# Kernel optimization log

Hardware: AMD Instinct MI355X
Metric: run time of the kernel (lower is better)

The kernel has to match this reference:

```python
import jax, jax.numpy as jnp
import numpy as np

V, D, MAXLEN, B, C = 32000, 1024, 2048, 4, 2048


def setup_inputs() -> dict:
    key = jax.random.key(0)
    ks = jax.random.split(key, 8)
    x = jax.random.randint(ks[0], (B, C), 0, V, dtype=jnp.int64)
    s = 0.02
    embed = jax.random.normal(ks[1], (V, D), dtype=jnp.float32) * s
    pe = jax.random.normal(ks[2], (MAXLEN, D), dtype=jnp.float32) * s
    Wq = jax.random.normal(ks[3], (D, D), dtype=jnp.float32) * s
    Wk = jax.random.normal(ks[4], (D, D), dtype=jnp.float32) * s
    Wv = jax.random.normal(ks[5], (D, D), dtype=jnp.float32) * s
    Wo = jax.random.normal(ks[6], (V, D), dtype=jnp.float32) * s
    bo = jnp.zeros((V,), dtype=jnp.float32)
    return {"x": x, "embed": embed, "pe": pe, "Wq": Wq, "Wk": Wk, "Wv": Wv, "Wo": Wo, "bo": bo}


def reference(x, embed, pe, Wq, Wk, Wv, Wo, bo):
    Bc, Cc = x.shape
    Dd = embed.shape[1]
    # token embedding + learned absolute PE (pos_offset = 0)
    h = embed[x] + pe[:Cc]                      # (B, C, D)
    # single-head Q/K/V projections (torch Linear: y = x @ W.T)
    Q = jnp.einsum('bcd,ed->bce', h, Wq)
    K = jnp.einsum('bcd,ed->bce', h, Wk)
    Vv = jnp.einsum('bcd,ed->bce', h, Wv)
    scores = jnp.einsum('bqd,bkd->bqk', Q, K) / jnp.sqrt(jnp.float32(Dd))
    # additive causal mask: 0 on lower triangle, -inf above
    mask = jnp.where(jnp.tril(jnp.ones((Cc, Cc), dtype=bool)), 0.0, -jnp.inf).astype(scores.dtype)
    weights = jax.nn.softmax(scores + mask, axis=-1)  # (B, C, C)
    attn_out = jnp.einsum('bqk,bkd->bqd', weights, Vv)
    hidden = h + attn_out
    logits = jnp.einsum('bcd,vd->bcv', hidden, Wo) + bo
    return logits
```

## Files before the change

### kernel.cpp

```cpp
#include <hip/hip_runtime.h>

#define DEV __device__ __forceinline__

typedef __attribute__((ext_vector_type(8))) __bf16 bf16x8;
typedef __attribute__((ext_vector_type(4))) float f32x4;

DEV unsigned short f2bf(float f) {
    unsigned u = __builtin_bit_cast(unsigned, f);
    u += 0x7fffu + ((u >> 16) & 1u);
    return (unsigned short)(u >> 16);
}
DEV float bf2f(unsigned short s) {
    unsigned u = ((unsigned)s) << 16;
    return __builtin_bit_cast(float, u);
}

DEV void gload_lds16(const unsigned short* g, unsigned short* l) {
    __builtin_amdgcn_global_load_lds(
        (const __attribute__((address_space(1))) unsigned int*)g,
        (__attribute__((address_space(3))) unsigned int*)l, 16, 0, 0);
}


__global__ __launch_bounds__(256) void k_cast_bf16(const float* __restrict__ src,
                                                   unsigned short* __restrict__ dst, int n4) {
    int i = blockIdx.x * 256 + threadIdx.x;
    if (i >= n4) return;
    float4 v = reinterpret_cast<const float4*>(src)[i];
    ushort4 o;
    o.x = f2bf(v.x); o.y = f2bf(v.y); o.z = f2bf(v.z); o.w = f2bf(v.w);
    reinterpret_cast<ushort4*>(dst)[i] = o;
}

__global__ __launch_bounds__(256) void k_cast3(const float* __restrict__ a,
                                               const float* __restrict__ b,
                                               const float* __restrict__ c,
                                               unsigned short* __restrict__ oa,
                                               unsigned short* __restrict__ ob,
                                               unsigned short* __restrict__ oc,
                                               int n4each) {
    int i = blockIdx.x * 256 + threadIdx.x;
    int w = i / n4each, j = i - w * n4each;
    const float* s = (w == 0) ? a : (w == 1) ? b : c;
    unsigned short* d = (w == 0) ? oa : (w == 1) ? ob : oc;
    float4 v = reinterpret_cast<const float4*>(s)[j];
    ushort4 o;
    o.x = f2bf(v.x); o.y = f2bf(v.y); o.z = f2bf(v.z); o.w = f2bf(v.w);
    reinterpret_cast<ushort4*>(d)[j] = o;
}

__global__ __launch_bounds__(256) void k_prep_h(const int* __restrict__ x,
                                                const float* __restrict__ embed,
                                                const float* __restrict__ pe,
                                                unsigned short* __restrict__ h) {
    const int r = blockIdx.x;
    const int pos = r & 2047;
    const int tok = x[r];
    const int t = threadIdx.x;
    float4 e = reinterpret_cast<const float4*>(embed + (size_t)tok * 1024)[t];
    float4 p = reinterpret_cast<const float4*>(pe + (size_t)pos * 1024)[t];
    ushort4 o;
    o.x = f2bf(e.x + p.x); o.y = f2bf(e.y + p.y);
    o.z = f2bf(e.z + p.z); o.w = f2bf(e.w + p.w);
    reinterpret_cast<ushort4*>(h + (size_t)r * 1024)[t] = o;
}

__global__ __launch_bounds__(256) void k_softmax_causal(const float* __restrict__ S,
                                                        unsigned short* __restrict__ W) {
    const int r = blockIdx.x;
    const int q = r & 2047;
    const float* row = S + (size_t)r * 2048;
    unsigned short* orow = W + (size_t)r * 2048;
    const int t = threadIdx.x;
    const float scale = 0.03125f;
    const int kceil4 = (((q >> 7) + 1) << 7) >> 2;
    float p[8];
    float mx = -1e30f;
    #pragma unroll
    for (int i = 0; i < 2; ++i) {
        int i4 = t + i * 256;
        int base = i4 * 4;
        float4 v = (float4){0.f, 0.f, 0.f, 0.f};
        if (base <= q) v = reinterpret_cast<const float4*>(row)[i4];
        p[i*4+0] = (base+0 <= q) ? v.x * scale : -1e30f;
        p[i*4+1] = (base+1 <= q) ? v.y * scale : -1e30f;
        p[i*4+2] = (base+2 <= q) ? v.z * scale : -1e30f;
        p[i*4+3] = (base+3 <= q) ? v.w * scale : -1e30f;
        #pragma unroll
        for (int j = 0; j < 4; ++j) mx = fmaxf(mx, p[i*4+j]);
    }
    #pragma unroll
    for (int o = 32; o > 0; o >>= 1) mx = fmaxf(mx, __shfl_xor(mx, o));
    __shared__ float redm[4];
    __shared__ float reds[4];
    const int w = t >> 6;
    if ((t & 63) == 0) redm[w] = mx;
    __syncthreads();
    mx = fmaxf(fmaxf(redm[0], redm[1]), fmaxf(redm[2], redm[3]));
    float e[8];
    float s = 0.f;
    #pragma unroll
    for (int i = 0; i < 8; ++i) { e[i] = __expf(p[i] - mx); s += e[i]; }
    #pragma unroll
    for (int o = 32; o > 0; o >>= 1) s += __shfl_xor(s, o);
    if ((t & 63) == 0) reds[w] = s;
    __syncthreads();
    s = (reds[0] + reds[1]) + (reds[2] + reds[3]);
    const float inv = 1.0f / s;
    #pragma unroll
    for (int i = 0; i < 2; ++i) {
        int i4 = t + i * 256;
        if (i4 < kceil4) {
            ushort4 o4;
            o4.x = f2bf(e[i*4+0] * inv);
            o4.y = f2bf(e[i*4+1] * inv);
            o4.z = f2bf(e[i*4+2] * inv);
            o4.w = f2bf(e[i*4+3] * inv);
            reinterpret_cast<ushort4*>(orow)[i4] = o4;
        }
    }
}

template<int OUT_BF16, int TRANS_OUT, int ADD_BIAS, int ADD_RES, int CAUSAL_SKIP, int TRI_K>
__global__ __launch_bounds__(256)
void k_gemm_bt(const unsigned short* __restrict__ A,
               const unsigned short* __restrict__ B,
               void* __restrict__ Out,
               const float* __restrict__ bias,
               const unsigned short* __restrict__ Res,
               int M, int N, int K, int ldo,
               long long sA, long long sB, long long sC, long long sRes) {
    const int bm = blockIdx.x, bn = blockIdx.y, bz = blockIdx.z;
    if (CAUSAL_SKIP && bn > bm) return;
    A += (long long)bz * sA;
    B += (long long)bz * sB;

    __shared__ __align__(16) unsigned short As[128 * 32];
    __shared__ __align__(16) unsigned short Bs[128 * 32];

    const int t = threadIdx.x;
    const int w = t >> 6;
    const int lane = t & 63;
    const int wm = w >> 1, wn = w & 1;
    const int fr = lane & 15, fq = lane >> 4;

    f32x4 acc[4][4];
    #pragma unroll
    for (int mi = 0; mi < 4; ++mi)
        #pragma unroll
        for (int ni = 0; ni < 4; ++ni)
            acc[mi][ni] = (f32x4){0.f, 0.f, 0.f, 0.f};

    const int kend = TRI_K ? ((K < (bm + 1) * 128) ? K : (bm + 1) * 128) : K;

    const int c0 = t, c1 = t + 256;
    const unsigned short* gA0 = A + (size_t)(bm * 128 + (c0 >> 2)) * K + (c0 & 3) * 8;
    const unsigned short* gA1 = A + (size_t)(bm * 128 + (c1 >> 2)) * K + (c1 & 3) * 8;
    const unsigned short* gB0 = B + (size_t)(bn * 128 + (c0 >> 2)) * K + (c0 & 3) * 8;
    const unsigned short* gB1 = B + (size_t)(bn * 128 + (c1 >> 2)) * K + (c1 & 3) * 8;
    unsigned short* lA0 = As + w * 512;
    unsigned short* lA1 = As + 2048 + w * 512;
    unsigned short* lB0 = Bs + w * 512;
    unsigned short* lB1 = Bs + 2048 + w * 512;

    for (int kt = 0; kt < kend; kt += 32) {
        gload_lds16(gA0 + kt, lA0);
        gload_lds16(gA1 + kt, lA1);
        gload_lds16(gB0 + kt, lB0);
        gload_lds16(gB1 + kt, lB1);
        __syncthreads();

        bf16x8 af[4], bfr[4];
        #pragma unroll
        for (int mi = 0; mi < 4; ++mi)
            af[mi] = *reinterpret_cast<const bf16x8*>(As + (wm * 64 + mi * 16 + fr) * 32 + fq * 8);
        #pragma unroll
        for (int ni = 0; ni < 4; ++ni)
            bfr[ni] = *reinterpret_cast<const bf16x8*>(Bs + (wn * 64 + ni * 16 + fr) * 32 + fq * 8);
        #pragma unroll
        for (int mi = 0; mi < 4; ++mi)
            #pragma unroll
            for (int ni = 0; ni < 4; ++ni)
                acc[mi][ni] = __builtin_amdgcn_mfma_f32_16x16x32_bf16(af[mi], bfr[ni], acc[mi][ni], 0, 0, 0);
        __syncthreads();
    }

    const int row0 = bm * 128 + wm * 64 + fq * 4;
    const int col0 = bn * 128 + wn * 64 + fr;
    if (OUT_BF16) {
        unsigned short* O = (unsigned short*)Out + (long long)bz * sC;
        #pragma unroll
        for (int mi = 0; mi < 4; ++mi) {
            #pragma unroll
            for (int j = 0; j < 4; ++j) {
                const int row = row0 + mi * 16 + j;
                unsigned short* orow = O + (size_t)row * ldo;
                const unsigned short* rrow =
                    ADD_RES ? (Res + (long long)bz * sRes + (size_t)row * ldo) : (const unsigned short*)nullptr;
                #pragma unroll
                for (int ni = 0; ni < 4; ++ni) {
                    const int col = col0 + ni * 16;
                    float v = acc[mi][ni][j];
                    if (ADD_RES) v += bf2f(rrow[col]);
                    orow[col] = f2bf(v);
                }
            }
        }
    } else {
        float* O = (float*)Out + (long long)bz * sC;
        #pragma unroll
        for (int mi = 0; mi < 4; ++mi) {
            #pragma unroll
            for (int j = 0; j < 4; ++j) {
                const int row = row0 + mi * 16 + j;
                float* orow = O + (size_t)row * ldo;
                #pragma unroll
                for (int ni = 0; ni < 4; ++ni) {
                    const int col = col0 + ni * 16;
                    float v = acc[mi][ni][j];
                    if (ADD_BIAS) v += bias[col];
                    orow[col] = v;
                }
            }
        }
    }
}


#define SA3(buf, kt) do { \
    unsigned short* d_ = Lds + (buf)*16384 + w*512; \
    gload_lds16(gA0 + (kt)*32, d_); \
    gload_lds16(gA1 + (kt)*32, d_ + 4096); } while(0)

#define SB3(buf, kt) do { \
    unsigned short* d_ = Lds + (buf)*16384 + 8192 + w*512; \
    gload_lds16(gB0 + (kt)*32, d_); \
    gload_lds16(gB1 + (kt)*32, d_ + 4096); } while(0)

#define LDA3(buf, mi) (*reinterpret_cast<const bf16x8*>(Lds + (buf)*16384 + aBase + (mi)*512))
#define LDB3(buf, ni) (*reinterpret_cast<const bf16x8*>(Lds + (buf)*16384 + 8192 + bBase + (ni)*512))

#define MF16(arow, af) do { \
    __builtin_amdgcn_s_setprio(1); \
    _Pragma("unroll") \
    for (int j_ = 0; j_ < 4; ++j_) \
        _Pragma("unroll") \
        for (int n_ = 0; n_ < 4; ++n_) \
            acc[(arow)+j_][n_] = __builtin_amdgcn_mfma_f32_16x16x32_bf16(af[j_], bb[n_], acc[(arow)+j_][n_], 0, 0, 0); \
    __builtin_amdgcn_s_setprio(0); } while(0)

#define BARX asm volatile("s_barrier" ::: "memory")

template<int EPI>
__global__ __launch_bounds__(512, 2)
void k_g256(const unsigned short* __restrict__ A,
            const unsigned short* __restrict__ B,
            void* __restrict__ O0, void* __restrict__ O1, void* __restrict__ O2,
            const float* __restrict__ bias) {
    constexpr int K = 1024;
    __shared__ __align__(16) unsigned short Lds[65536];

    int bm, bn, bz = 0;
    if (EPI == 2) {
        bm = blockIdx.x; bn = blockIdx.y; bz = blockIdx.z;
        if (bn > bm) return;
    } else {
        int wg = blockIdx.x;
        wg = (wg & 7) * 48 + (wg >> 3);
        bm = wg % 32; bn = wg / 32;
    }

    const unsigned short* Ab = A + (EPI == 2 ? (size_t)bz * 2048 * K : 0);
    const unsigned short* Bb2 = B + (EPI == 2 ? (size_t)bz * 2048 * K : 0);

    const int tid = threadIdx.x;
    const int w = tid >> 6, lane = tid & 63;
    const int wm = w >> 2, wn = w & 3;
    const int fr = lane & 15, fq = lane >> 4;
    const int sl = fq ^ ((fr >> 1) & 3);

    const int c0 = w * 64 + lane, c1 = c0 + 512;
    const int r0 = c0 >> 2, s0 = ((c0 & 3) ^ ((r0 >> 1) & 3)) * 8;
    const int r1 = c1 >> 2, s1 = ((c1 & 3) ^ ((r1 >> 1) & 3)) * 8;
    const unsigned short* gA0 = Ab + (size_t)(bm * 256 + r0) * K + s0;
    const unsigned short* gA1 = Ab + (size_t)(bm * 256 + r1) * K + s1;
    const unsigned short* gB0 = Bb2 + (size_t)(bn * 256 + r0) * K + s0;
    const unsigned short* gB1 = Bb2 + (size_t)(bn * 256 + r1) * K + s1;

    const int aBase = (wm * 128 + fr) * 32 + sl * 8;
    const int bBase = (wn * 64 + fr) * 32 + sl * 8;

    f32x4 acc[8][4];
    #pragma unroll
    for (int i = 0; i < 8; ++i)
        #pragma unroll
        for (int j = 0; j < 4; ++j)
            acc[i][j] = (f32x4){0.f, 0.f, 0.f, 0.f};

    SA3(0, 0); SB3(0, 0);
    SA3(1, 1); SB3(1, 1);
    SA3(2, 2); SB3(2, 2);
    asm volatile("s_waitcnt vmcnt(8)" ::: "memory");
    BARX;
    bf16x8 a0[4], bb[4];
    #pragma unroll
    for (int j = 0; j < 4; ++j) a0[j] = LDA3(0, j);
    #pragma unroll
    for (int j = 0; j < 4; ++j) bb[j] = LDB3(0, j);

    #pragma unroll
    for (int t = 0; t < 32; ++t) {
        const int bc = t & 3, b1 = (t + 1) & 3, bs = (t + 3) & 3;
        const int ks = (t + 3) & 31;
        bf16x8 a1t[4];
        #pragma unroll
        for (int j = 0; j < 4; ++j) a1t[j] = LDA3(bc, 4 + j);
        SA3(bs, ks);
        BARX;
        MF16(0, a0);
        asm volatile("s_waitcnt vmcnt(6)" ::: "memory");
        BARX;
        bf16x8 a0n[4], bn_[4];
        #pragma unroll
        for (int j = 0; j < 4; ++j) a0n[j] = LDA3(b1, j);
        #pragma unroll
        for (int j = 0; j < 4; ++j) bn_[j] = LDB3(b1, j);
        SB3(bs, ks);
        BARX;
        MF16(4, a1t);
        BARX;
        #pragma unroll
        for (int j = 0; j < 4; ++j) { a0[j] = a0n[j]; bb[j] = bn_[j]; }
    }
    asm volatile("s_waitcnt vmcnt(0)" ::: "memory");

    const int row0 = bm * 256 + wm * 128 + fq * 4;
    const int col0 = bn * 256 + wn * 64 + fr;
    if (EPI == 1) {
        if (bn < 8) {
            unsigned short* O = (unsigned short*)(bn < 4 ? O0 : O1);
            const int cb = (bn < 4) ? 0 : 1024;
            #pragma unroll
            for (int mi = 0; mi < 8; ++mi) {
                #pragma unroll
                for (int j = 0; j < 4; ++j) {
                    unsigned short* orow = O + (size_t)(row0 + mi * 16 + j) * 1024;
                    #pragma unroll
                    for (int ni = 0; ni < 4; ++ni)
                        orow[col0 + ni * 16 - cb] = f2bf(acc[mi][ni][j]);
                }
            }
        } else {
            unsigned short* O = (unsigned short*)O2 + (size_t)(row0 >> 11) * 2097152;
            const int i0 = row0 & 2047;
            #pragma unroll
            for (int mi = 0; mi < 8; ++mi) {
                #pragma unroll
                for (int ni = 0; ni < 4; ++ni) {
                    const int e = col0 + ni * 16 - 2048;
                    ushort4 o4;
                    o4.x = f2bf(acc[mi][ni][0]);
                    o4.y = f2bf(acc[mi][ni][1]);
                    o4.z = f2bf(acc[mi][ni][2]);
                    o4.w = f2bf(acc[mi][ni][3]);
                    *reinterpret_cast<ushort4*>(O + (size_t)e * 2048 + i0 + mi * 16) = o4;
                }
            }
        }
    } else {
        float* Out = (float*)O0 + (size_t)bz * 2048 * 2048;
        #pragma unroll
        for (int mi = 0; mi < 8; ++mi) {
            #pragma unroll
            for (int j = 0; j < 4; ++j) {
                float* orow = Out + (size_t)(row0 + mi * 16 + j) * 2048;
                #pragma unroll
                for (int ni = 0; ni < 4; ++ni)
                    orow[col0 + ni * 16] = acc[mi][ni][j];
            }
        }
    }
}


__global__ __launch_bounds__(512, 2)
void k_glog2(const unsigned short* __restrict__ A,
             const unsigned short* __restrict__ B,
             float* __restrict__ Out,
             const float* __restrict__ bias) {
    constexpr int K = 1024;
    __shared__ __align__(16) unsigned short Lds[65536];

    int wg = blockIdx.x;
    wg = (wg & 7) * 500 + (wg >> 3);
    const int tb = wg / 20, u = wg % 20;
    const int bm = (tb & 7) * 4 + (u & 3);
    const int bn = (tb >> 3) * 5 + (u >> 2);

    const int tid = threadIdx.x;
    const int w = tid >> 6, lane = tid & 63;
    const int wm = w >> 2, wn = w & 3;
    const int fr = lane & 15, fq = lane >> 4;
    const int sl = fq ^ ((fr >> 1) & 3);

    const int c0 = w * 64 + lane, c1 = c0 + 512;
    const int r0 = c0 >> 2, s0 = ((c0 & 3) ^ ((r0 >> 1) & 3)) * 8;
    const int r1 = c1 >> 2, s1 = ((c1 & 3) ^ ((r1 >> 1) & 3)) * 8;
    const unsigned short* gA0 = A + (size_t)(bm * 256 + r0) * K + s0;
    const unsigned short* gA1 = A + (size_t)(bm * 256 + r1) * K + s1;
    const unsigned short* gB0 = B + (size_t)(bn * 256 + r0) * K + s0;
    const unsigned short* gB1 = B + (size_t)(bn * 256 + r1) * K + s1;

    const int aBase = (wm * 128 + fr) * 32 + sl * 8;
    const int bBase = (wn * 64 + fr) * 32 + sl * 8;

    f32x4 acc[8][4];
    #pragma unroll
    for (int i = 0; i < 8; ++i)
        #pragma unroll
        for (int j = 0; j < 4; ++j)
            acc[i][j] = (f32x4){0.f, 0.f, 0.f, 0.f};

    SA3(0, 0); SB3(0, 0);
    SA3(1, 1); SB3(1, 1);
    SA3(2, 2); SB3(2, 2);
    asm volatile("s_waitcnt vmcnt(8)" ::: "memory");
    BARX;

    #pragma unroll
    for (int t = 0; t < 32; ++t) {
        const int bc = t & 3, bs = (t + 3) & 3;
        const int ks = (t + 3) & 31;
        SA3(bs, ks);
        SB3(bs, ks);
        bf16x8 af[8], bf_[4];
        #pragma unroll
        for (int mi = 0; mi < 8; ++mi) af[mi] = LDA3(bc, mi);
        #pragma unroll
        for (int ni = 0; ni < 4; ++ni) bf_[ni] = LDB3(bc, ni);
        __builtin_amdgcn_s_setprio(1);
        #pragma unroll
        for (int mi = 0; mi < 8; ++mi)
            #pragma unroll
            for (int ni = 0; ni < 4; ++ni)
                acc[mi][ni] = __builtin_amdgcn_mfma_f32_16x16x32_bf16(af[mi], bf_[ni], acc[mi][ni], 0, 0, 0);
        __builtin_amdgcn_s_setprio(0);
        asm volatile("s_waitcnt vmcnt(8)" ::: "memory");
        BARX;
    }
    asm volatile("s_waitcnt vmcnt(0)" ::: "memory");

    const int row0 = bm * 256 + wm * 128 + fq * 4;
    const int col0 = bn * 256 + wn * 64 + fr;
    float bia[4];
    #pragma unroll
    for (int ni = 0; ni < 4; ++ni) bia[ni] = bias[col0 + ni * 16];
    #pragma unroll
    for (int mi = 0; mi < 8; ++mi) {
        #pragma unroll
        for (int j = 0; j < 4; ++j) {
            float* orow = Out + (size_t)(row0 + mi * 16 + j) * 32000;
            #pragma unroll
            for (int ni = 0; ni < 4; ++ni)
                orow[col0 + ni * 16] = acc[mi][ni][j] + bia[ni];
        }
    }
    asm volatile("s_waitcnt vmcnt(0)" ::: "memory");
}


extern "C" void kernel_launch(void* const* d_in, const int* in_sizes, int n_in,
                              void* d_out, int out_size, void* d_ws, size_t ws_size,
                              hipStream_t stream) {
    (void)in_sizes; (void)n_in; (void)out_size; (void)ws_size;
    constexpr int Bb = 4, Cc = 2048, Dd = 1024, Vv = 32000;
    constexpr int M = Bb * Cc;

    const int*   x     = (const int*)d_in[0];
    const float* embed = (const float*)d_in[1];
    const float* pe    = (const float*)d_in[2];
    const float* Wq    = (const float*)d_in[3];
    const float* Wk    = (const float*)d_in[4];
    const float* Wv    = (const float*)d_in[5];
    const float* Wo    = (const float*)d_in[6];
    const float* bo    = (const float*)d_in[7];
    float* out = (float*)d_out;

    char* p = (char*)d_ws;
    auto au = [&](size_t n) { unsigned short* r = (unsigned short*)p; p += n * sizeof(unsigned short); return r; };
    unsigned short* h_bf   = au((size_t)M * Dd);
    unsigned short* hid_bf = au((size_t)M * Dd);
    unsigned short* Qb     = au((size_t)M * Dd);
    unsigned short* Kb     = au((size_t)M * Dd);
    unsigned short* Vt     = au((size_t)M * Dd);
    unsigned short* Wqb    = au((size_t)Dd * Dd);
    unsigned short* Wkb    = au((size_t)Dd * Dd);
    unsigned short* Wvb    = au((size_t)Dd * Dd);
    unsigned short* Wob    = au((size_t)Vv * Dd);
    unsigned short* Wt     = au((size_t)Bb * Cc * Cc);
    float* Sc = (float*)p;

    k_cast3<<<dim3(3 * Dd * Dd / 4 / 256), 256, 0, stream>>>(Wq, Wk, Wv, Wqb, Wkb, Wvb, Dd * Dd / 4);
    k_cast_bf16<<<dim3(Vv * Dd / 4 / 256), 256, 0, stream>>>(Wo, Wob, Vv * Dd / 4);
    k_prep_h<<<dim3(M), 256, 0, stream>>>(x, embed, pe, h_bf);

    k_g256<1><<<dim3(384), 512, 0, stream>>>(h_bf, Wqb, Qb, Kb, Vt, nullptr);

    k_g256<2><<<dim3(8, 8, 4), 512, 0, stream>>>(Qb, Kb, Sc, nullptr, nullptr, nullptr);

    k_softmax_causal<<<dim3(M), 256, 0, stream>>>(Sc, Wt);

    {
        dim3 g(Cc / 128, Dd / 128, Bb);
        k_gemm_bt<1,0,0,1,0,1><<<g, 256, 0, stream>>>(Wt, Vt, hid_bf, nullptr, h_bf,
            Cc, Dd, Cc, Dd, (long long)Cc * Cc, (long long)Dd * Cc, (long long)Cc * Dd, (long long)Cc * Dd);
    }

    k_glog2<<<dim3(4000), 512, 0, stream>>>(hid_bf, Wob, out, bo);
}
```

Measured before the change: 801.6 us.

## Make logits GEMM blocks loop over four M tiles with cross-tile prefetch

The output-projection GEMM now launches 1000 blocks instead of 4000. Each block walks four consecutive 256-row M tiles for a fixed N tile. During the last K steps of one tile it prefetches the first K slices of the next tile into LDS, so the fp32 epilogue stores overlap with the next tile's loads. The bias is loaded once per block. In exchange the grid becomes coarser, which can worsen wave-tail balance. It also drops the previous 2D swizzle used for L2 locality of A tiles.

```diff
diff --git a/kernel.cpp b/kernel.cpp
--- a/kernel.cpp
+++ b/kernel.cpp
@@ -232,6 +232,11 @@
     gload_lds16(gA0 + (kt)*32, d_); \
     gload_lds16(gA1 + (kt)*32, d_ + 4096); } while(0)
 
+#define SA3n(buf, kt) do { \
+    unsigned short* d_ = Lds + (buf)*16384 + w*512; \
+    gload_lds16(nA0 + (kt)*32, d_); \
+    gload_lds16(nA1 + (kt)*32, d_ + 4096); } while(0)
+
 #define SB3(buf, kt) do { \
     unsigned short* d_ = Lds + (buf)*16384 + 8192 + w*512; \
     gload_lds16(gB0 + (kt)*32, d_); \
@@ -384,7 +389,7 @@
 
 
 __global__ __launch_bounds__(512, 2)
-void k_glog2(const unsigned short* __restrict__ A,
+void k_glogP(const unsigned short* __restrict__ A,
              const unsigned short* __restrict__ B,
              float* __restrict__ Out,
              const float* __restrict__ bias) {
@@ -392,10 +397,9 @@
     __shared__ __align__(16) unsigned short Lds[65536];
 
     int wg = blockIdx.x;
-    wg = (wg & 7) * 500 + (wg >> 3);
-    const int tb = wg / 20, u = wg % 20;
-    const int bm = (tb & 7) * 4 + (u & 3);
-    const int bn = (tb >> 3) * 5 + (u >> 2);
+    wg = (wg & 7) * 125 + (wg >> 3);
+    const int bq = wg & 7;
+    const int bn = wg >> 3;
 
     const int tid = threadIdx.x;
     const int w = tid >> 6, lane = tid & 63;
@@ -406,8 +410,9 @@
     const int c0 = w * 64 + lane, c1 = c0 + 512;
     const int r0 = c0 >> 2, s0 = ((c0 & 3) ^ ((r0 >> 1) & 3)) * 8;
     const int r1 = c1 >> 2, s1 = ((c1 & 3) ^ ((r1 >> 1) & 3)) * 8;
-    const unsigned short* gA0 = A + (size_t)(bm * 256 + r0) * K + s0;
-    const unsigned short* gA1 = A + (size_t)(bm * 256 + r1) * K + s1;
+    const long long segStride = (long long)256 * K;
+    const unsigned short* gA0 = A + (size_t)(bq * 1024 + r0) * K + s0;
+    const unsigned short* gA1 = A + (size_t)(bq * 1024 + r1) * K + s1;
     const unsigned short* gB0 = B + (size_t)(bn * 256 + r0) * K + s0;
     const unsigned short* gB1 = B + (size_t)(bn * 256 + r1) * K + s1;
 
@@ -420,6 +425,11 @@
         #pragma unroll
         for (int j = 0; j < 4; ++j)
             acc[i][j] = (f32x4){0.f, 0.f, 0.f, 0.f};
+
+    const int col0 = bn * 256 + wn * 64 + fr;
+    float bia[4];
+    #pragma unroll
+    for (int ni = 0; ni < 4; ++ni) bia[ni] = bias[col0 + ni * 16];
 
     SA3(0, 0); SB3(0, 0);
     SA3(1, 1); SB3(1, 1);
@@ -427,45 +437,66 @@
     asm volatile("s_waitcnt vmcnt(8)" ::: "memory");
     BARX;
 
-    #pragma unroll
-    for (int t = 0; t < 32; ++t) {
-        const int bc = t & 3, bs = (t + 3) & 3;
-        const int ks = (t + 3) & 31;
-        SA3(bs, ks);
-        SB3(bs, ks);
-        bf16x8 af[8], bf_[4];
-        #pragma unroll
-        for (int mi = 0; mi < 8; ++mi) af[mi] = LDA3(bc, mi);
-        #pragma unroll
-        for (int ni = 0; ni < 4; ++ni) bf_[ni] = LDB3(bc, ni);
-        __builtin_amdgcn_s_setprio(1);
-        #pragma unroll
-        for (int mi = 0; mi < 8; ++mi)
-            #pragma unroll
-            for (int ni = 0; ni < 4; ++ni)
-                acc[mi][ni] = __builtin_amdgcn_mfma_f32_16x16x32_bf16(af[mi], bf_[ni], acc[mi][ni], 0, 0, 0);
-        __builtin_amdgcn_s_setprio(0);
-        asm volatile("s_waitcnt vmcnt(8)" ::: "memory");
-        BARX;
-    }
-    asm volatile("s_waitcnt vmcnt(0)" ::: "memory");
-
-    const int row0 = bm * 256 + wm * 128 + fq * 4;
-    const int col0 = bn * 256 + wn * 64 + fr;
-    float bia[4];
-    #pragma unroll
-    for (int ni = 0; ni < 4; ++ni) bia[ni] = bias[col0 + ni * 16];
-    #pragma unroll
-    for (int mi = 0; mi < 8; ++mi) {
-        #pragma unroll
-        for (int j = 0; j < 4; ++j) {
-            float* orow = Out + (size_t)(row0 + mi * 16 + j) * 32000;
-            #pragma unroll
-            for (int ni = 0; ni < 4; ++ni)
-                orow[col0 + ni * 16] = acc[mi][ni][j] + bia[ni];
-        }
-    }
-    asm volatile("s_waitcnt vmcnt(0)" ::: "memory");
+    for (int s = 0; s < 4; ++s) {
+        const unsigned short* nA0 = gA0 + segStride;
+        const unsigned short* nA1 = gA1 + segStride;
+        const bool more = (s < 3);
+
+        #pragma unroll
+        for (int t = 0; t < 32; ++t) {
+            const int bc = t & 3, bs = (t + 3) & 3;
+            if (t < 29) {
+                SA3(bs, t + 3);
+                SB3(bs, t + 3);
+            } else if (more) {
+                SA3n(bs, t - 29);
+                SB3(bs, t - 29);
+            }
+            bf16x8 af[8], bf_[4];
+            #pragma unroll
+            for (int mi = 0; mi < 8; ++mi) af[mi] = LDA3(bc, mi);
+            #pragma unroll
+            for (int ni = 0; ni < 4; ++ni) bf_[ni] = LDB3(bc, ni);
+            __builtin_amdgcn_s_setprio(1);
+            #pragma unroll
+            for (int mi = 0; mi < 8; ++mi)
+                #pragma unroll
+                for (int ni = 0; ni < 4; ++ni)
+                    acc[mi][ni] = __builtin_amdgcn_mfma_f32_16x16x32_bf16(af[mi], bf_[ni], acc[mi][ni], 0, 0, 0);
+            __builtin_amdgcn_s_setprio(0);
+            if (t < 29 || more) {
+                asm volatile("s_waitcnt vmcnt(8)" ::: "memory");
+            } else if (t == 29) {
+                asm volatile("s_waitcnt vmcnt(4)" ::: "memory");
+            } else if (t == 30) {
+                asm volatile("s_waitcnt vmcnt(0)" ::: "memory");
+            }
+            if (t < 31) BARX;
+        }
+
+        const int row0 = (bq * 4 + s) * 256 + wm * 128 + fq * 4;
+        #pragma unroll
+        for (int mi = 0; mi < 8; ++mi) {
+            #pragma unroll
+            for (int j = 0; j < 4; ++j) {
+                float* orow = Out + (size_t)(row0 + mi * 16 + j) * 32000;
+                #pragma unroll
+                for (int ni = 0; ni < 4; ++ni)
+                    orow[col0 + ni * 16] = acc[mi][ni][j] + bia[ni];
+            }
+        }
+
+        if (more) {
+            asm volatile("s_waitcnt vmcnt(63)" ::: "memory");
+            BARX;
+            #pragma unroll
+            for (int i = 0; i < 8; ++i)
+                #pragma unroll
+                for (int j = 0; j < 4; ++j)
+                    acc[i][j] = (f32x4){0.f, 0.f, 0.f, 0.f};
+            gA0 = nA0; gA1 = nA1;
+        }
+    }
 }
 
 
@@ -516,5 +547,5 @@
             Cc, Dd, Cc, Dd, (long long)Cc * Cc, (long long)Dd * Cc, (long long)Cc * Dd, (long long)Cc * Dd);
     }
 
-    k_glog2<<<dim3(4000), 512, 0, stream>>>(hid_bf, Wob, out, bo);
-}
+    k_glogP<<<dim3(1000), 512, 0, stream>>>(hid_bf, Wob, out, bo);
+}
```

After: 1.258 ms, median of 2. +57.0%, slower.

## Load logits GEMM B operand directly from global into registers, bypassing LDS

Applied to the files above, without the earlier changes.

The final vocab-projection GEMM now stages only the A tile (hidden states) in LDS through async global-to-LDS loads. Each wave reads its B fragments (Wo rows) straight from global memory into registers, prefetched one k-step ahead. This halves LDS footprint and LDS read traffic, which could allow higher occupancy. In exchange the B loads are no longer shared across the waves of a block, so redundant global/L2 traffic increases. The vmcnt wait counts were also adjusted, and they are fragile.

```diff
diff --git a/kernel.cpp b/kernel.cpp
--- a/kernel.cpp
+++ b/kernel.cpp
@@ -383,13 +383,20 @@
 }
 
 
+#define SAO(buf, kt) do { \
+    unsigned short* d_ = LdsA + (buf)*8192 + w*512; \
+    gload_lds16(gA0 + (kt)*32, d_); \
+    gload_lds16(gA1 + (kt)*32, d_ + 4096); } while(0)
+
+#define LDAO(buf, mi) (*reinterpret_cast<const bf16x8*>(LdsA + (buf)*8192 + aBase + (mi)*512))
+
 __global__ __launch_bounds__(512, 2)
-void k_glog2(const unsigned short* __restrict__ A,
+void k_glogB(const unsigned short* __restrict__ A,
              const unsigned short* __restrict__ B,
              float* __restrict__ Out,
              const float* __restrict__ bias) {
     constexpr int K = 1024;
-    __shared__ __align__(16) unsigned short Lds[65536];
+    __shared__ __align__(16) unsigned short LdsA[32768];
 
     int wg = blockIdx.x;
     wg = (wg & 7) * 500 + (wg >> 3);
@@ -408,11 +415,13 @@
     const int r1 = c1 >> 2, s1 = ((c1 & 3) ^ ((r1 >> 1) & 3)) * 8;
     const unsigned short* gA0 = A + (size_t)(bm * 256 + r0) * K + s0;
     const unsigned short* gA1 = A + (size_t)(bm * 256 + r1) * K + s1;
-    const unsigned short* gB0 = B + (size_t)(bn * 256 + r0) * K + s0;
-    const unsigned short* gB1 = B + (size_t)(bn * 256 + r1) * K + s1;
 
     const int aBase = (wm * 128 + fr) * 32 + sl * 8;
-    const int bBase = (wn * 64 + fr) * 32 + sl * 8;
+
+    const unsigned short* gB[4];
+    #pragma unroll
+    for (int ni = 0; ni < 4; ++ni)
+        gB[ni] = B + (size_t)(bn * 256 + wn * 64 + ni * 16 + fr) * K + fq * 8;
 
     f32x4 acc[8][4];
     #pragma unroll
@@ -421,31 +430,40 @@
         for (int j = 0; j < 4; ++j)
             acc[i][j] = (f32x4){0.f, 0.f, 0.f, 0.f};
 
-    SA3(0, 0); SB3(0, 0);
-    SA3(1, 1); SB3(1, 1);
-    SA3(2, 2); SB3(2, 2);
-    asm volatile("s_waitcnt vmcnt(8)" ::: "memory");
+    bf16x8 cb[4], nb[4];
+
+    #pragma unroll
+    for (int ni = 0; ni < 4; ++ni) nb[ni] = *reinterpret_cast<const bf16x8*>(gB[ni]);
+    SAO(0, 0);
+    SAO(1, 1);
+    SAO(2, 2);
+    asm volatile("s_waitcnt vmcnt(4)" ::: "memory");
     BARX;
+    #pragma unroll
+    for (int ni = 0; ni < 4; ++ni) cb[ni] = nb[ni];
 
     #pragma unroll
     for (int t = 0; t < 32; ++t) {
         const int bc = t & 3, bs = (t + 3) & 3;
+        const int kn = ((t + 1) & 31) * 32;
         const int ks = (t + 3) & 31;
-        SA3(bs, ks);
-        SB3(bs, ks);
-        bf16x8 af[8], bf_[4];
-        #pragma unroll
-        for (int mi = 0; mi < 8; ++mi) af[mi] = LDA3(bc, mi);
-        #pragma unroll
-        for (int ni = 0; ni < 4; ++ni) bf_[ni] = LDB3(bc, ni);
+        #pragma unroll
+        for (int ni = 0; ni < 4; ++ni)
+            nb[ni] = *reinterpret_cast<const bf16x8*>(gB[ni] + kn);
+        SAO(bs, ks);
+        bf16x8 af[8];
+        #pragma unroll
+        for (int mi = 0; mi < 8; ++mi) af[mi] = LDAO(bc, mi);
         __builtin_amdgcn_s_setprio(1);
         #pragma unroll
         for (int mi = 0; mi < 8; ++mi)
             #pragma unroll
             for (int ni = 0; ni < 4; ++ni)
-                acc[mi][ni] = __builtin_amdgcn_mfma_f32_16x16x32_bf16(af[mi], bf_[ni], acc[mi][ni], 0, 0, 0);
+                acc[mi][ni] = __builtin_amdgcn_mfma_f32_16x16x32_bf16(af[mi], cb[ni], acc[mi][ni], 0, 0, 0);
         __builtin_amdgcn_s_setprio(0);
-        asm volatile("s_waitcnt vmcnt(8)" ::: "memory");
+        asm volatile("s_waitcnt vmcnt(2)" ::: "memory");
+        #pragma unroll
+        for (int ni = 0; ni < 4; ++ni) cb[ni] = nb[ni];
         BARX;
     }
     asm volatile("s_waitcnt vmcnt(0)" ::: "memory");
@@ -516,5 +534,5 @@
             Cc, Dd, Cc, Dd, (long long)Cc * Cc, (long long)Dd * Cc, (long long)Cc * Dd, (long long)Cc * Dd);
     }
 
-    k_glog2<<<dim3(4000), 512, 0, stream>>>(hid_bf, Wob, out, bo);
-}
+    k_glogB<<<dim3(4000), 512, 0, stream>>>(hid_bf, Wob, out, bo);
+}
```

After: 1.051 ms. 1.31x slower.
